# Optimization experiments

Measured on AMD Instinct MI355X. Metric: run time of the kernel, lower is better.

The kernel has to match this reference:

```python
import jax, jax.numpy as jnp
import numpy as np

B, S, HID = 2, 2048, 2048
H, HKV = 16, 4
D = HID // H          # 128
N_REP = H // HKV      # 4
ROPE_THETA = 1000000.0


def _rope_tables(seq_len, head_dim, theta):
    inv_freq = 1.0 / (theta ** (jnp.arange(0, head_dim, 2, dtype=jnp.float32) / head_dim))
    freqs = jnp.arange(seq_len, dtype=jnp.float32)[:, None] * inv_freq[None, :]  # [S, D/2]
    emb = jnp.concatenate([freqs, freqs], axis=-1)  # [S, D]
    return jnp.cos(emb), jnp.sin(emb)


def setup_inputs() -> dict:
    key = jax.random.key(0)
    ks = jax.random.split(key, 6)
    cos, sin = _rope_tables(S, D, ROPE_THETA)
    sc = 0.02
    return {
        "x": jax.random.normal(ks[0], (B, S, HID), jnp.float32),
        "cos": cos,
        "sin": sin,
        "Wq": jax.random.normal(ks[1], (HID, H * D), jnp.float32) * sc,
        "Wk": jax.random.normal(ks[2], (HID, HKV * D), jnp.float32) * sc,
        "Wv": jax.random.normal(ks[3], (HID, HKV * D), jnp.float32) * sc,
        "Wo": jax.random.normal(ks[4], (H * D, HID), jnp.float32) * sc,
    }


def _rotate_half(t):
    t1, t2 = jnp.split(t, 2, axis=-1)
    return jnp.concatenate([-t2, t1], axis=-1)


def reference(x, cos, sin, Wq, Wk, Wv, Wo):
    b, s, _ = x.shape
    q = (x @ Wq).reshape(b, s, H, D)    # [b,s,H,d]
    k = (x @ Wk).reshape(b, s, HKV, D)  # [b,s,Hkv,d]
    v = (x @ Wv).reshape(b, s, HKV, D)

    # RoPE (cos/sin broadcast over head axis)
    c = cos[:s, None, :]  # [s,1,d]
    sn = sin[:s, None, :]
    q = q * c + _rotate_half(q) * sn
    k = k * c + _rotate_half(k) * sn

    # GQA: repeat kv heads (interleaved, matching repeat_kv)
    k = jnp.repeat(k, N_REP, axis=2)  # [b,s,H,d]
    v = jnp.repeat(v, N_REP, axis=2)

    q = q.transpose(0, 2, 1, 3)  # [b,H,s,d]
    k = k.transpose(0, 2, 1, 3)
    v = v.transpose(0, 2, 1, 3)

    scale = 1.0 / jnp.sqrt(jnp.asarray(D, x.dtype))
    scores = jnp.einsum("bhqd,bhkd->bhqk", q, k) * scale
    causal = jnp.tril(jnp.ones((s, s), dtype=bool))
    scores = jnp.where(causal[None, None], scores, jnp.asarray(-jnp.inf, scores.dtype))
    probs = jax.nn.softmax(scores, axis=-1)
    out = jnp.einsum("bhqk,bhkd->bhqd", probs, v)
    out = out.transpose(0, 2, 1, 3).reshape(b, s, H * D)
    return out @ Wo
```

## Files before the change

### kernel.cpp

```cpp
#include <hip/hip_runtime.h>
#include <cstdint>

#define B_    2
#define S_    2048
#define HID_  2048
#define H_    16
#define HKV_  4
#define D_    128
#define SCALE_ 0.08838834764831845f
#define LOG2E_ 1.4426950408889634f
#define K1_   (SCALE_ * LOG2E_)
#define THRS_ 62.75f

typedef __bf16 bf16x8 __attribute__((ext_vector_type(8)));
typedef float  f32x4  __attribute__((ext_vector_type(4)));
typedef int    intx2  __attribute__((ext_vector_type(2)));
using u16 = unsigned short;

static __device__ __forceinline__ u16 f2bf(float f) {
  union { float f; uint32_t u; } c; c.f = f;
  uint32_t u = c.u;
  return (u16)((u + 0x7FFFu + ((u >> 16) & 1u)) >> 16);
}
static __device__ __forceinline__ float bf2f(u16 h) {
  union { uint32_t u; float f; } c; c.u = ((uint32_t)h) << 16;
  return c.f;
}
static __device__ __forceinline__ void async16(const u16* g, u16* lds) {
  __builtin_amdgcn_global_load_lds((const __attribute__((address_space(1))) void*)g,
                                   (__attribute__((address_space(3))) void*)lds, 16, 0, 0);
}

__global__ void cast_f32_bf16(const float* __restrict__ in, u16* __restrict__ out, int n4) {
  int i = blockIdx.x * blockDim.x + threadIdx.x;
  if (i < n4) {
    float4 v = ((const float4*)in)[i];
    ushort4 o;
    o.x = f2bf(v.x); o.y = f2bf(v.y); o.z = f2bf(v.z); o.w = f2bf(v.w);
    ((ushort4*)out)[i] = o;
  }
}

__global__ __launch_bounds__(256) void transpose_cast_all(const float* __restrict__ Wq,
                                                          const float* __restrict__ Wk,
                                                          const float* __restrict__ Wv,
                                                          const float* __restrict__ Wo,
                                                          u16* __restrict__ Wt,
                                                          u16* __restrict__ Wot) {
  __shared__ float tile[32][33];
  const int tx = threadIdx.x, ty = threadIdx.y;
  const int t = blockIdx.x;
  const float* W; u16* Dst; int N, lt;
  if (t < 4096)      { W = Wq; Dst = Wt;                        N = 2048; lt = t; }
  else if (t < 5120) { W = Wk; Dst = Wt + (size_t)2048 * 2048;  N = 512;  lt = t - 4096; }
  else if (t < 6144) { W = Wv; Dst = Wt + (size_t)2560 * 2048;  N = 512;  lt = t - 5120; }
  else               { W = Wo; Dst = Wot;                       N = 2048; lt = t - 6144; }
  const int tn = N >> 5;
  const int n0 = (lt % tn) * 32, k0 = (lt / tn) * 32;
#pragma unroll
  for (int j = 0; j < 32; j += 8)
    tile[ty + j][tx] = W[(size_t)(k0 + ty + j) * N + n0 + tx];
  __syncthreads();
#pragma unroll
  for (int j = 0; j < 32; j += 8)
    Dst[(size_t)(n0 + ty + j) * 2048 + k0 + tx] = f2bf(tile[tx][ty + j]);
}

__global__ __launch_bounds__(256) void v_transpose(const u16* __restrict__ qkv,
                                                   u16* __restrict__ Vt) {
  __shared__ u16 tile[32][34];
  const int tx = threadIdx.x, ty = threadIdx.y;
  const int mat = blockIdx.z;
  const int b = mat >> 2, kv = mat & 3;
  const int d0 = blockIdx.x * 32, s0 = blockIdx.y * 32;
#pragma unroll
  for (int j = 0; j < 32; j += 8)
    tile[ty + j][tx] = qkv[(size_t)(b * S_ + s0 + ty + j) * 3072 + 2560 + kv * 128 + d0 + tx];
  __syncthreads();
#pragma unroll
  for (int j = 0; j < 32; j += 8)
    Vt[((size_t)mat * D_ + d0 + ty + j) * S_ + s0 + tx] = tile[tx][ty + j];
}

template<int BF16OUT>
__global__ __launch_bounds__(256, 4) void gemm_bt(const u16* __restrict__ A,
                                                  const u16* __restrict__ Bt,
                                                  void* __restrict__ Cv,
                                                  int M, int N, int K, int gx) {
  const int nwg = (int)gridDim.x;
  const int bid = (int)blockIdx.x;
  const int qq = nwg >> 3, rr = nwg & 7;
  const int xcd = bid & 7, pos = bid >> 3;
  const int wg = ((xcd < rr) ? xcd * (qq + 1) : rr * (qq + 1) + (xcd - rr) * qq) + pos;
  const int bm = (wg % gx) * 128;
  const int bn = (wg / gx) * 128;

  __shared__ __align__(16) u16 Ash[128 * 64];
  __shared__ __align__(16) u16 Bsh[128 * 64];
  const int tid = threadIdx.x;
  const int w = tid >> 6, l = tid & 63;
  const int wm = (w >> 1) * 64, wn = (w & 1) * 64;

  const f32x4 z4 = {0.f, 0.f, 0.f, 0.f};
  f32x4 acc[4][4];
#pragma unroll
  for (int i = 0; i < 4; ++i)
#pragma unroll
    for (int j = 0; j < 4; ++j) acc[i][j] = z4;

  const int srow = w * 8 + (l >> 3);
  const int schunk = l & 7;

  for (int k0 = 0; k0 < K; k0 += 64) {
#pragma unroll
    for (int i = 0; i < 4; ++i) {
      const int row = i * 32 + srow;
      const int ch = schunk ^ (row & 7);
      async16(A + (size_t)(bm + row) * K + k0 + ch * 8, &Ash[(i * 4 + w) * 512]);
      async16(Bt + (size_t)(bn + row) * K + k0 + ch * 8, &Bsh[(i * 4 + w) * 512]);
    }
    asm volatile("s_waitcnt vmcnt(0)" ::: "memory");
    __syncthreads();
#pragma unroll
    for (int kc = 0; kc < 2; ++kc) {
      bf16x8 af[4], bfr[4];
#pragma unroll
      for (int mi = 0; mi < 4; ++mi) {
        const int r = wm + mi * 16 + (l & 15);
        const int c2 = (kc * 4 + (l >> 4)) ^ (r & 7);
        af[mi] = *(const bf16x8*)&Ash[r * 64 + c2 * 8];
      }
#pragma unroll
      for (int ni = 0; ni < 4; ++ni) {
        const int r = wn + ni * 16 + (l & 15);
        const int c2 = (kc * 4 + (l >> 4)) ^ (r & 7);
        bfr[ni] = *(const bf16x8*)&Bsh[r * 64 + c2 * 8];
      }
#pragma unroll
      for (int mi = 0; mi < 4; ++mi)
#pragma unroll
        for (int ni = 0; ni < 4; ++ni)
          acc[mi][ni] = __builtin_amdgcn_mfma_f32_16x16x32_bf16(af[mi], bfr[ni], acc[mi][ni], 0, 0, 0);
    }
    __syncthreads();
  }
#pragma unroll
  for (int mi = 0; mi < 4; ++mi) {
    const int r0 = bm + wm + mi * 16 + ((l >> 4) << 2);
#pragma unroll
    for (int ni = 0; ni < 4; ++ni) {
      const int c = bn + wn + ni * 16 + (l & 15);
#pragma unroll
      for (int j = 0; j < 4; ++j) {
        if (BF16OUT) ((u16*)Cv)[(size_t)(r0 + j) * N + c] = f2bf(acc[mi][ni][j]);
        else         ((float*)Cv)[(size_t)(r0 + j) * N + c] = acc[mi][ni][j];
      }
    }
  }
}

__global__ void rope_scatter(const u16* __restrict__ qkv,
                             const float* __restrict__ cosb, const float* __restrict__ sinb,
                             u16* __restrict__ Qr, u16* __restrict__ Kr) {
  const int NQ = B_ * S_ * H_ * 64;
  const int NK = B_ * S_ * HKV_ * 64;
  const int idx = blockIdx.x * 256 + threadIdx.x;
  if (idx < NQ) {
    const int j = idx & 63, rest = idx >> 6;
    const int h = rest & 15, srow = rest >> 4;
    const int s = srow & (S_ - 1);
    const u16* base = qkv + (size_t)srow * 3072 + h * 128;
    const float c = cosb[s * 128 + j], sn = sinb[s * 128 + j];
    const float a = bf2f(base[j]), b2 = bf2f(base[j + 64]);
    const size_t qo = (((size_t)(srow >> 11) * H_ + h) * S_ + s) * D_;
    Qr[qo + j]      = f2bf(a * c - b2 * sn);
    Qr[qo + j + 64] = f2bf(b2 * c + a * sn);
  } else if (idx < NQ + NK) {
    const int t = idx - NQ;
    const int j = t & 63, rest = t >> 6;
    const int kv = rest & 3, srow = rest >> 2;
    const int s = srow & (S_ - 1);
    const u16* base = qkv + (size_t)srow * 3072 + 2048 + kv * 128;
    const float c = cosb[s * 128 + j], sn = sinb[s * 128 + j];
    const float a = bf2f(base[j]), b2 = bf2f(base[j + 64]);
    const size_t ko = (((size_t)(srow >> 11) * HKV_ + kv) * S_ + s) * D_;
    Kr[ko + j]      = f2bf(a * c - b2 * sn);
    Kr[ko + j + 64] = f2bf(b2 * c + a * sn);
  }
}

__global__ __launch_bounds__(256, 3) void attn_kernel(const u16* __restrict__ Q,
                                                      const u16* __restrict__ Kc,
                                                      const u16* __restrict__ Vt,
                                                      u16* __restrict__ O) {
  const int bid = blockIdx.x;
  const int bh  = bid & 31;
  const int qt  = 31 - (bid >> 5);
  const int b   = bh >> 4;
  const int kvh = (bh & 15) >> 2;
  const int tid = threadIdx.x;
  const int w = tid >> 6, l = tid & 63;
  const int g = l >> 4, c = l & 15;
  const int q0 = qt * 64;

  __shared__ __align__(16) u16 Ksh[64 * 128];
  __shared__ __align__(16) u16 Vsh[128 * 64];

  const u16* Kbase = Kc + ((size_t)(b * HKV_ + kvh) * S_) * D_;
  const u16* Vbase = Vt + ((size_t)(b * HKV_ + kvh) * D_) * S_;

  bf16x8 qf[4];
  {
    const u16* qp = Q + ((size_t)bh * S_ + q0 + w * 16 + c) * D_ + g * 8;
#pragma unroll
    for (int kc = 0; kc < 4; ++kc) qf[kc] = *(const bf16x8*)(qp + kc * 32);
  }

  int srcK[4], srcV[4];
#pragma unroll
  for (int i = 0; i < 4; ++i) {
    const int rK = i * 16 + w * 4 + g;
    srcK[i] = rK * 128 + (c ^ (rK & 7)) * 8;
    const int dV = i * 32 + w * 8 + (l >> 3);
    srcV[i] = dV * S_ + ((l & 7) ^ (dV & 7)) * 8;
  }

  const f32x4 z4 = {0.f, 0.f, 0.f, 0.f};
  f32x4 oacc[8];
#pragma unroll
  for (int nb = 0; nb < 8; ++nb) oacc[nb] = z4;
  float m_i = -1e30f, l_i = 0.f;

  auto stage = [&](int kv0) {
#pragma unroll
    for (int i = 0; i < 4; ++i) {
      async16(Kbase + (size_t)kv0 * 128 + srcK[i], &Ksh[i * 2048 + w * 512]);
      async16(Vbase + kv0 + srcV[i],               &Vsh[i * 2048 + w * 512]);
    }
  };

  const uint32_t voff = (uint32_t)(c * 128 + (((g >> 1) ^ (c & 7)) << 4) + ((g & 1) << 3));

  const int nt = qt + 1;
  for (int t = 0; t < nt; ++t) {
    const int kv0 = t << 6;
    if (t) __syncthreads();
    stage(kv0);
    asm volatile("s_waitcnt vmcnt(0)" ::: "memory");
    __syncthreads();

    f32x4 sf[4];
#pragma unroll
    for (int nb = 0; nb < 4; ++nb) sf[nb] = z4;

    __builtin_amdgcn_s_setprio(1);
#pragma unroll
    for (int kc = 0; kc < 4; ++kc) {
#pragma unroll
      for (int nb = 0; nb < 4; ++nb) {
        const int r = nb * 16 + c;
        const int s2 = (kc * 4 + g) ^ (c & 7);
        const bf16x8 kf = *(const bf16x8*)&Ksh[r * 128 + s2 * 8];
        sf[nb] = __builtin_amdgcn_mfma_f32_16x16x32_bf16(kf, qf[kc], sf[nb], 0, 0, 0);
      }
    }
    __builtin_amdgcn_s_setprio(0);

    {
      const int qcol = q0 + w * 16 + c;
      const bool doMask = (t == nt - 1);
      float mx = -3e38f;
#pragma unroll
      for (int nb = 0; nb < 4; ++nb)
#pragma unroll
        for (int jj = 0; jj < 4; ++jj) {
          float sv = sf[nb][jj];
          if (doMask) {
            const int kk = kv0 + nb * 16 + g * 4 + jj;
            sv = (kk > qcol) ? -3e38f : sv;
            sf[nb][jj] = sv;
          }
          mx = fmaxf(mx, sv);
        }
      mx = fmaxf(mx, __shfl_xor(mx, 16));
      mx = fmaxf(mx, __shfl_xor(mx, 32));

      if (__all(mx <= m_i + THRS_)) {
        const float mk = m_i * K1_;
        float rs = 0.f;
#pragma unroll
        for (int nb = 0; nb < 4; ++nb)
#pragma unroll
          for (int jj = 0; jj < 4; ++jj) {
            const float p = exp2f(fmaf(sf[nb][jj], K1_, -mk));
            sf[nb][jj] = p;
            rs += p;
          }
        rs += __shfl_xor(rs, 16);
        rs += __shfl_xor(rs, 32);
        l_i += rs;
      } else {
        const float mnew = fmaxf(m_i, mx);
        const float fsc = exp2f((m_i - mnew) * K1_);
        m_i = mnew;
        const float mk = mnew * K1_;
        float rs = 0.f;
#pragma unroll
        for (int nb = 0; nb < 4; ++nb)
#pragma unroll
          for (int jj = 0; jj < 4; ++jj) {
            const float p = exp2f(fmaf(sf[nb][jj], K1_, -mk));
            sf[nb][jj] = p;
            rs += p;
          }
        rs += __shfl_xor(rs, 16);
        rs += __shfl_xor(rs, 32);
        l_i = l_i * fsc + rs;
        float fq[4];
#pragma unroll
        for (int j = 0; j < 4; ++j) fq[j] = __shfl(fsc, g * 4 + j);
#pragma unroll
        for (int nb = 0; nb < 8; ++nb)
#pragma unroll
          for (int j = 0; j < 4; ++j) oacc[nb][j] *= fq[j];
      }
    }

    bf16x8 pa, pb;
#pragma unroll
    for (int jj = 0; jj < 4; ++jj) {
      pa[jj] = (__bf16)sf[0][jj]; pa[4 + jj] = (__bf16)sf[1][jj];
      pb[jj] = (__bf16)sf[2][jj]; pb[4 + jj] = (__bf16)sf[3][jj];
    }

    __builtin_amdgcn_s_setprio(1);
#pragma unroll
    for (int kc2 = 0; kc2 < 2; ++kc2) {
      const bf16x8 pfr = kc2 ? pb : pa;
      const uint32_t vk = voff ^ (uint32_t)(kc2 << 6);
#pragma unroll
      for (int nb = 0; nb < 8; ++nb) {
        union { intx2 h[2]; bf16x8 v; } u_;
        u_.h[0] = *(const intx2*)((const char*)Vsh + (vk + nb * 2048));
        u_.h[1] = *(const intx2*)((const char*)Vsh + ((vk ^ 32u) + nb * 2048));
        oacc[nb] = __builtin_amdgcn_mfma_f32_16x16x32_bf16(pfr, u_.v, oacc[nb], 0, 0, 0);
      }
    }
    __builtin_amdgcn_s_setprio(0);
  }

#pragma unroll
  for (int j = 0; j < 4; ++j) {
    const float li = __shfl(l_i, g * 4 + j);
    const float inv = 1.f / li;
    const int srow = q0 + w * 16 + g * 4 + j;
    u16* op = O + ((size_t)(b * S_ + srow)) * HID_ + (bh & 15) * D_ + c;
#pragma unroll
    for (int nb = 0; nb < 8; ++nb) op[nb * 16] = f2bf(oacc[nb][j] * inv);
  }
}

extern "C" void kernel_launch(void* const* d_in, const int* in_sizes, int n_in,
                              void* d_out, int out_size, void* d_ws, size_t ws_size,
                              hipStream_t stream) {
  const float* x    = (const float*)d_in[0];
  const float* cosb = (const float*)d_in[1];
  const float* sinb = (const float*)d_in[2];
  const float* Wq   = (const float*)d_in[3];
  const float* Wk   = (const float*)d_in[4];
  const float* Wv   = (const float*)d_in[5];
  const float* Wo   = (const float*)d_in[6];
  float* out = (float*)d_out;

  u16*   xb   = (u16*)d_ws;
  u16*   Wt   = xb  + (size_t)4096 * 2048;
  u16*   Wot  = Wt  + (size_t)3072 * 2048;
  u16*   qkv  = Wot + (size_t)2048 * 2048;
  u16*   Qr   = qkv + (size_t)4096 * 3072;
  u16*   Kr   = Qr  + (size_t)B_ * H_ * S_ * D_;
  u16*   Vtb  = Kr  + (size_t)B_ * HKV_ * S_ * D_;
  u16*   Ob   = Vtb + (size_t)B_ * HKV_ * S_ * D_;

  cast_f32_bf16<<<8192, 256, 0, stream>>>(x, xb, (B_ * S_ * HID_) / 4);

  dim3 tb(32, 8);
  transpose_cast_all<<<dim3(10240), tb, 0, stream>>>(Wq, Wk, Wv, Wo, Wt, Wot);

  gemm_bt<1><<<dim3(768), 256, 0, stream>>>(xb, Wt, qkv, 4096, 3072, 2048, 32);

  rope_scatter<<<20480, 256, 0, stream>>>(qkv, cosb, sinb, Qr, Kr);
  v_transpose<<<dim3(4, 64, 8), tb, 0, stream>>>(qkv, Vtb);

  attn_kernel<<<dim3(1024), 256, 0, stream>>>(Qr, Kr, Vtb, Ob);

  gemm_bt<0><<<dim3(512), 256, 0, stream>>>(Ob, Wot, out, 4096, 2048, 2048, 32);
}
```

Before: 222.3 us.

## Prefetch next K/V tiles during attention compute and permute Vt for 128-bit LDS reads

The attention loop now double-buffers V in LDS and issues the next tile's V load before QK^T and the next K load after it, so global-to-LDS traffic overlaps with MFMA and softmax work instead of stalling at the top of every iteration. The V transpose kernel writes keys in a permuted order within each 64-key block. This lets the PV MFMA read its B operand as one contiguous 16-byte LDS load rather than two 8-byte loads. The cost is a doubled V LDS footprint and an extra barrier per iteration, which may reduce occupancy at 3 blocks per CU.

```diff
diff --git a/kernel.cpp b/kernel.cpp
--- a/kernel.cpp
+++ b/kernel.cpp
@@ -14,7 +14,6 @@
 
 typedef __bf16 bf16x8 __attribute__((ext_vector_type(8)));
 typedef float  f32x4  __attribute__((ext_vector_type(4)));
-typedef int    intx2  __attribute__((ext_vector_type(2)));
 using u16 = unsigned short;
 
 static __device__ __forceinline__ u16 f2bf(float f) {
@@ -77,9 +76,13 @@
   for (int j = 0; j < 32; j += 8)
     tile[ty + j][tx] = qkv[(size_t)(b * S_ + s0 + ty + j) * 3072 + 2560 + kv * 128 + d0 + tx];
   __syncthreads();
+  const int sc  = s0 + tx;
+  const int t64 = sc & 63;
+  const int p   = ((t64 >> 5) * 4 + ((t64 >> 2) & 3)) * 8 + ((t64 >> 4) & 1) * 4 + (t64 & 3);
+  const int scp = (sc & ~63) | p;
 #pragma unroll
   for (int j = 0; j < 32; j += 8)
-    Vt[((size_t)mat * D_ + d0 + ty + j) * S_ + s0 + tx] = tile[tx][ty + j];
+    Vt[((size_t)mat * D_ + d0 + ty + j) * S_ + scp] = tile[tx][ty + j];
 }
 
 template<int BF16OUT>
@@ -204,7 +207,7 @@
   const int q0 = qt * 64;
 
   __shared__ __align__(16) u16 Ksh[64 * 128];
-  __shared__ __align__(16) u16 Vsh[128 * 64];
+  __shared__ __align__(16) u16 VshF[2 * 128 * 64];
 
   const u16* Kbase = Kc + ((size_t)(b * HKV_ + kvh) * S_) * D_;
   const u16* Vbase = Vt + ((size_t)(b * HKV_ + kvh) * D_) * S_;
@@ -231,23 +234,26 @@
   for (int nb = 0; nb < 8; ++nb) oacc[nb] = z4;
   float m_i = -1e30f, l_i = 0.f;
 
-  auto stage = [&](int kv0) {
-#pragma unroll
-    for (int i = 0; i < 4; ++i) {
+  auto stageK = [&](int kv0) {
+#pragma unroll
+    for (int i = 0; i < 4; ++i)
       async16(Kbase + (size_t)kv0 * 128 + srcK[i], &Ksh[i * 2048 + w * 512]);
-      async16(Vbase + kv0 + srcV[i],               &Vsh[i * 2048 + w * 512]);
-    }
   };
-
-  const uint32_t voff = (uint32_t)(c * 128 + (((g >> 1) ^ (c & 7)) << 4) + ((g & 1) << 3));
+  auto stageV = [&](int buf, int kv0) {
+#pragma unroll
+    for (int i = 0; i < 4; ++i)
+      async16(Vbase + kv0 + srcV[i], &VshF[buf * 8192 + i * 2048 + w * 512]);
+  };
 
   const int nt = qt + 1;
+  stageV(0, 0);
+  stageK(0);
+
   for (int t = 0; t < nt; ++t) {
-    const int kv0 = t << 6;
-    if (t) __syncthreads();
-    stage(kv0);
+    const int cur = t & 1;
     asm volatile("s_waitcnt vmcnt(0)" ::: "memory");
     __syncthreads();
+    if (t + 1 < nt) stageV(cur ^ 1, (t + 1) << 6);
 
     f32x4 sf[4];
 #pragma unroll
@@ -266,7 +272,11 @@
     }
     __builtin_amdgcn_s_setprio(0);
 
+    __syncthreads();
+    if (t + 1 < nt) stageK((t + 1) << 6);
+
     {
+      const int kv0 = t << 6;
       const int qcol = q0 + w * 16 + c;
       const bool doMask = (t == nt - 1);
       float mx = -3e38f;
@@ -333,17 +343,16 @@
       pb[jj] = (__bf16)sf[2][jj]; pb[4 + jj] = (__bf16)sf[3][jj];
     }
 
+    const char* Vb = (const char*)&VshF[cur * 8192] + c * 128;
     __builtin_amdgcn_s_setprio(1);
 #pragma unroll
     for (int kc2 = 0; kc2 < 2; ++kc2) {
       const bf16x8 pfr = kc2 ? pb : pa;
-      const uint32_t vk = voff ^ (uint32_t)(kc2 << 6);
+      const int s2v = ((kc2 * 4 + g) ^ (c & 7)) << 4;
 #pragma unroll
       for (int nb = 0; nb < 8; ++nb) {
-        union { intx2 h[2]; bf16x8 v; } u_;
-        u_.h[0] = *(const intx2*)((const char*)Vsh + (vk + nb * 2048));
-        u_.h[1] = *(const intx2*)((const char*)Vsh + ((vk ^ 32u) + nb * 2048));
-        oacc[nb] = __builtin_amdgcn_mfma_f32_16x16x32_bf16(pfr, u_.v, oacc[nb], 0, 0, 0);
+        const bf16x8 vf = *(const bf16x8*)(Vb + nb * 2048 + s2v);
+        oacc[nb] = __builtin_amdgcn_mfma_f32_16x16x32_bf16(pfr, vf, oacc[nb], 0, 0, 0);
       }
     }
     __builtin_amdgcn_s_setprio(0);
```

New measurement: 201.5 us. 1.1x faster.
